# Kernel optimization log

Measured on AMD Instinct MI355X. Metric: run time of the kernel, lower is better.

Reference implementation:

```python
import jax, jax.numpy as jnp
import numpy as np

# Grid / acquisition constants (see input_specs)
NY = NX = 384
NS, NSRC, NREC, NT = 4, 1, 96, 600
DX, DT = 4.0, 0.0005          # from init_kwargs
MAX_VEL = 2500.0              # max_vel passed to scalar()
PML_WIDTH = 20                # PML absorbing-layer width in cells


def setup_inputs() -> dict:
    key = jax.random.key(0)
    k1, k2, k3, k4 = jax.random.split(key, 4)
    # velocity model in [1500, 2500] m/s (consistent with max_vel=2500)
    vp = 1500.0 + 1000.0 * jax.random.uniform(k1, (NY, NX), dtype=jnp.float32)
    src_amp_y = jax.random.normal(k2, (NS, NSRC, NT), dtype=jnp.float32)
    # locations kept inside the interior, away from the PML
    src_loc_y = jax.random.randint(k3, (NS, NSRC, 2), PML_WIDTH + 10, NY - PML_WIDTH - 10).astype(jnp.int32)
    rec_loc_y = jax.random.randint(k4, (NS, NREC, 2), PML_WIDTH + 10, NY - PML_WIDTH - 10).astype(jnp.int32)
    return {"vp": vp, "src_amp_y": src_amp_y, "src_loc_y": src_loc_y, "rec_loc_y": rec_loc_y}


def _pml_sigma_1d(n):
    # quadratic PML damping profile, classic 3*vmax*ln(1000)/(2*L) scaling
    x = jnp.arange(n, dtype=jnp.float32)
    left = jnp.clip((PML_WIDTH - x) / PML_WIDTH, 0.0)
    right = jnp.clip((x - (n - 1 - PML_WIDTH)) / PML_WIDTH, 0.0)
    d0 = 3.0 * MAX_VEL * np.log(1000.0) / (2.0 * PML_WIDTH * DX)
    return d0 * jnp.maximum(left, right) ** 2


def _laplacian(u):
    # 4th-order accurate 2D Laplacian, zero (Dirichlet) padding; u: [S, ny, nx]
    c0, c1, c2 = -1.0 / 12.0, 4.0 / 3.0, -5.0 / 2.0
    up = jnp.pad(u, ((0, 0), (2, 2), (2, 2)))
    ly = (c0 * (up[:, :-4, 2:-2] + up[:, 4:, 2:-2])
          + c1 * (up[:, 1:-3, 2:-2] + up[:, 3:-1, 2:-2])
          + c2 * up[:, 2:-2, 2:-2])
    lx = (c0 * (up[:, 2:-2, :-4] + up[:, 2:-2, 4:])
          + c1 * (up[:, 2:-2, 1:-3] + up[:, 2:-2, 3:-1])
          + c2 * up[:, 2:-2, 2:-2])
    return (ly + lx) / (DX * DX)


def _propagate(vp, src_amp_y, src_loc_y, rec_loc_y):
    S = src_amp_y.shape[0]
    v2dt2 = (vp * vp) * (DT * DT)                     # [ny, nx]
    sigma = _pml_sigma_1d(NY)[:, None] + _pml_sigma_1d(NX)[None, :]
    a = 1.0 + 0.5 * DT * sigma                        # damped leapfrog denominators
    b = 1.0 - 0.5 * DT * sigma

    sy, sx = src_loc_y[..., 0], src_loc_y[..., 1]     # [S, nsrc]
    ry, rx = rec_loc_y[..., 0], rec_loc_y[..., 1]     # [S, nrec]
    shot_s = jnp.broadcast_to(jnp.arange(S)[:, None], sy.shape)
    shot_r = jnp.broadcast_to(jnp.arange(S)[:, None], ry.shape)
    src_scale = v2dt2[sy, sx]                         # [S, nsrc]

    def step(carry, amp_t):
        u_prev, u_cur = carry
        lap = _laplacian(u_cur)
        u_next = (2.0 * u_cur - b * u_prev + v2dt2 * lap) / a
        u_next = u_next.at[shot_s, sy, sx].add(amp_t * src_scale)
        rec = u_next[shot_r, ry, rx]                  # [S, nrec]
        return (u_cur, u_next), rec

    u0 = jnp.zeros((S, NY, NX), dtype=vp.dtype)
    amp_ts = jnp.transpose(src_amp_y, (2, 0, 1))      # [nt, S, nsrc]
    _, recs = jax.lax.scan(step, (u0, u0), amp_ts)
    return jnp.transpose(recs, (1, 2, 0))             # [S, nrec, nt]


def reference(vp, src_amp_y, src_loc_y, rec_loc_y):
    return _propagate(vp, src_amp_y, src_loc_y, rec_loc_y)
```

## Files before the change

kernel.cpp:

```cpp
#include <hip/hip_runtime.h>

constexpr int NY = 384, NX = 384, S = 4, NREC = 96, NT = 600;
constexpr int K = 8;
constexpr int T = 48;
constexpr int L = 80;
constexpr int PAD = 16;
constexpr int PX = NX + 2 * PAD;
constexpr int PNN = PX * PX;
constexpr int TB = NX / T;
constexpr int SP = 84;
constexpr int NPAIR = (L / 2) * (L / 4);
constexpr int TPB = 512;
constexpr float D0 = 323.80102870228766f;
constexpr float HALF_DT = 0.00025f;
constexpr float DT2 = 2.5e-7f;
constexpr float C0 = -1.0f / 12.0f, C1 = 4.0f / 3.0f, C2 = -2.5f;
constexpr float INV_DX2 = 0.0625f;

__device__ __forceinline__ float sigma_of(int y, int x) {
    float yf = (float)y, xf = (float)x;
    float a = fmaxf((20.0f - yf) / 20.0f, 0.0f);
    float b = fmaxf((yf - 363.0f) / 20.0f, 0.0f);
    float m = fmaxf(a, b);
    float sy = D0 * m * m;
    a = fmaxf((20.0f - xf) / 20.0f, 0.0f);
    b = fmaxf((xf - 363.0f) / 20.0f, 0.0f);
    m = fmaxf(a, b);
    float sx = D0 * m * m;
    return sy + sx;
}

__global__ __launch_bounds__(256) void init_vp(
    const float* __restrict__ vp, float* __restrict__ vppad)
{
    int i = blockIdx.x * 256 + threadIdx.x;
    if (i >= PNN) return;
    int py = i / PX, px = i - py * PX;
    int dy = py - PAD, dx = px - PAD;
    bool in = ((unsigned)dy < (unsigned)NY) && ((unsigned)dx < (unsigned)NX);
    vppad[i] = in ? vp[dy * NX + dx] : 0.0f;
}

__device__ __forceinline__ float4 ld4g(const float* p) { return *(const float4*)p; }
__device__ __forceinline__ void st4g(float* p, float4 v) { *(float4*)p = v; }
__device__ __forceinline__ float get4(const float4& v, int c) {
    return c == 0 ? v.x : c == 1 ? v.y : c == 2 ? v.z : v.w;
}
__device__ __forceinline__ void set4(float4& v, int c, float x) {
    if (c == 0) v.x = x; else if (c == 1) v.y = x; else if (c == 2) v.z = x; else v.w = x;
}

__device__ __forceinline__ void coeff_quad(int gy, int gx, float4 vq,
                                           float4& v2, float4& bb, float4& ia)
{
    v2.x = vq.x * vq.x * DT2; v2.y = vq.y * vq.y * DT2;
    v2.z = vq.z * vq.z * DT2; v2.w = vq.w * vq.w * DT2;
    float s0 = sigma_of(gy, gx),     s1 = sigma_of(gy, gx + 1);
    float s2 = sigma_of(gy, gx + 2), s3 = sigma_of(gy, gx + 3);
    bb.x = 1.0f - HALF_DT * s0; bb.y = 1.0f - HALF_DT * s1;
    bb.z = 1.0f - HALF_DT * s2; bb.w = 1.0f - HALF_DT * s3;
    float a0 = 1.0f + HALF_DT * s0, a1 = 1.0f + HALF_DT * s1;
    float a2 = 1.0f + HALF_DT * s2, a3 = 1.0f + HALF_DT * s3;
    bool iny = ((unsigned)gy < (unsigned)NY);
    ia.x = (iny && (unsigned)gx < (unsigned)NX)       ? 1.0f / a0 : 0.0f;
    ia.y = (iny && (unsigned)(gx + 1) < (unsigned)NX) ? 1.0f / a1 : 0.0f;
    ia.z = (iny && (unsigned)(gx + 2) < (unsigned)NX) ? 1.0f / a2 : 0.0f;
    ia.w = (iny && (unsigned)(gx + 3) < (unsigned)NX) ? 1.0f / a3 : 0.0f;
}

__device__ __forceinline__ float4 quad_update(
    float4 cen, float4 up, float4 v2, float4 bb, float4 ia,
    float4 ym2, float4 ym1, float4 yp1, float4 yp2,
    float xm2a, float xm1a, float xp1a, float xp2a)
{
    float4 r;
    float lyv, lxv, lap;
    lyv = C0 * (ym2.x + yp2.x) + C1 * (ym1.x + yp1.x) + C2 * cen.x;
    lxv = C0 * (xm2a + cen.z) + C1 * (xm1a + cen.y) + C2 * cen.x;
    lap = (lyv + lxv) * INV_DX2;
    r.x = (2.0f * cen.x - bb.x * up.x + v2.x * lap) * ia.x;
    lyv = C0 * (ym2.y + yp2.y) + C1 * (ym1.y + yp1.y) + C2 * cen.y;
    lxv = C0 * (xm1a + cen.w) + C1 * (cen.x + cen.z) + C2 * cen.y;
    lap = (lyv + lxv) * INV_DX2;
    r.y = (2.0f * cen.y - bb.y * up.y + v2.y * lap) * ia.y;
    lyv = C0 * (ym2.z + yp2.z) + C1 * (ym1.z + yp1.z) + C2 * cen.z;
    lxv = C0 * (cen.x + xp1a) + C1 * (cen.y + cen.w) + C2 * cen.z;
    lap = (lyv + lxv) * INV_DX2;
    r.z = (2.0f * cen.z - bb.z * up.z + v2.z * lap) * ia.z;
    lyv = C0 * (ym2.w + yp2.w) + C1 * (ym1.w + yp1.w) + C2 * cen.w;
    lxv = C0 * (cen.y + xp2a) + C1 * (cen.z + xp1a) + C2 * cen.w;
    lap = (lyv + lxv) * INV_DX2;
    r.w = (2.0f * cen.w - bb.w * up.w + v2.w * lap) * ia.w;
    return r;
}

__device__ __forceinline__ void pair_step(
    const float* __restrict__ Ain, float* __restrict__ Aout,
    int m, int rl, int qc4, float aj,
    float4& cenL, float4& cenU, float4& upL, float4& upU,
    const float4& v2L, const float4& v2U, const float4& bbL, const float4& bbU,
    const float4& iaL, const float4& iaU, const float4& saL, const float4& saU)
{
    if (rl < m || rl >= L - m || qc4 + 3 < m || qc4 >= L - m) return;
    const int b = rl * SP + qc4;
    float4 rm2 = *(const float4*)&Ain[b - 2 * SP];
    float4 rm1 = *(const float4*)&Ain[b - SP];
    float4 rp2 = *(const float4*)&Ain[b + 2 * SP];
    float4 rp3 = *(const float4*)&Ain[b + 3 * SP];
    float2 xmL = *(const float2*)&Ain[b - 2];
    float2 xpL = *(const float2*)&Ain[b + 4];
    float2 xmU = *(const float2*)&Ain[b + SP - 2];
    float2 xpU = *(const float2*)&Ain[b + SP + 4];
    float4 rL = quad_update(cenL, upL, v2L, bbL, iaL, rm2, rm1, cenU, rp2,
                            xmL.x, xmL.y, xpL.x, xpL.y);
    float4 rU = quad_update(cenU, upU, v2U, bbU, iaU, rm1, cenL, rp2, rp3,
                            xmU.x, xmU.y, xpU.x, xpU.y);
    rL.x += aj * saL.x; rL.y += aj * saL.y; rL.z += aj * saL.z; rL.w += aj * saL.w;
    rU.x += aj * saU.x; rU.y += aj * saU.y; rU.z += aj * saU.z; rU.w += aj * saU.w;
    *(float4*)&Aout[b] = rL;
    *(float4*)&Aout[b + SP] = rU;
    upL = cenL; cenL = rL;
    upU = cenU; cenU = rU;
}

__device__ __forceinline__ void slot_setup(
    int p, int py0, int px0, int gy0, int gx0, int sly, int slx, bool has_src,
    const float* __restrict__ upIn, const float* __restrict__ ucIn,
    const float* __restrict__ vppad, float* __restrict__ A0,
    int& rl, int& qc4,
    float4& cenL, float4& cenU, float4& upL, float4& upU,
    float4& v2L, float4& v2U, float4& bbL, float4& bbU,
    float4& iaL, float4& iaU, float4& saL, float4& saU)
{
    int pr = p / 20;
    qc4 = (p - pr * 20) * 4;
    rl = 2 * pr;
    int pa = (py0 + rl) * PX + px0 + qc4;
    upL = ld4g(upIn + pa);        upU = ld4g(upIn + pa + PX);
    cenL = ld4g(ucIn + pa);       cenU = ld4g(ucIn + pa + PX);
    *(float4*)&A0[rl * SP + qc4] = cenL;
    *(float4*)&A0[(rl + 1) * SP + qc4] = cenU;
    float4 vqL = ld4g(vppad + pa), vqU = ld4g(vppad + pa + PX);
    int gy = gy0 + rl, gx = gx0 + qc4;
    coeff_quad(gy,     gx, vqL, v2L, bbL, iaL);
    coeff_quad(gy + 1, gx, vqU, v2U, bbU, iaU);
    saL = make_float4(0.f, 0.f, 0.f, 0.f); saU = saL;
    if (has_src && slx >= qc4 && slx < qc4 + 4) {
        int c = slx - qc4;
        if (sly == rl)          set4(saL, c, get4(v2L, c));
        else if (sly == rl + 1) set4(saU, c, get4(v2U, c));
    }
}

__global__ __launch_bounds__(TPB) void stepK(
    float* __restrict__ ubuf,
    const float* __restrict__ vppad,
    const float* __restrict__ src_amp,
    const int* __restrict__ src_loc,
    const int* __restrict__ rec_loc,
    float* __restrict__ out,
    int t0, int pin, int pout)
{
    __shared__ __align__(16) float A0[SP * L];
    __shared__ __align__(16) float A1[SP * L];
    __shared__ int r_lidx[NREC];
    __shared__ int r_tout[NREC];
    __shared__ int r_cnt;

    const int tid = threadIdx.x;
    const int bx = blockIdx.x, by = blockIdx.y, s = blockIdx.z;

    const float* upIn = ubuf + (size_t)(s * 4 + pin) * PNN;
    const float* ucIn = upIn + PNN;
    float* upOut = ubuf + (size_t)(s * 4 + pout) * PNN;
    float* ucOut = upOut + PNN;

    const int py0 = by * T;
    const int px0 = bx * T;
    const int gy0 = py0 - PAD;
    const int gx0 = px0 - PAD;

    if (tid == 0) r_cnt = 0;

    const int sy = src_loc[2 * s], sx = src_loc[2 * s + 1];
    const int sly = sy - gy0, slx = sx - gx0;
    const bool has_src = ((unsigned)sly < (unsigned)L) && ((unsigned)slx < (unsigned)L);
    const float4 a0 = ld4g(&src_amp[s * NT + t0]);
    const float4 a1 = ld4g(&src_amp[s * NT + t0 + 4]);

    const bool act1 = (tid < NPAIR - TPB);
    int rl0, qc40, rl1 = 2, qc41 = 0;
    float4 cenL0, cenU0, upL0, upU0, v2L0, v2U0, bbL0, bbU0, iaL0, iaU0, saL0, saU0;
    float4 cenL1 = {}, cenU1 = {}, upL1 = {}, upU1 = {}, v2L1 = {}, v2U1 = {},
           bbL1 = {}, bbU1 = {}, iaL1 = {}, iaU1 = {}, saL1 = {}, saU1 = {};

    slot_setup(tid, py0, px0, gy0, gx0, sly, slx, has_src, upIn, ucIn, vppad, A0,
               rl0, qc40, cenL0, cenU0, upL0, upU0, v2L0, v2U0, bbL0, bbU0,
               iaL0, iaU0, saL0, saU0);
    if (act1)
        slot_setup(tid + TPB, py0, px0, gy0, gx0, sly, slx, has_src, upIn, ucIn, vppad, A0,
                   rl1, qc41, cenL1, cenU1, upL1, upU1, v2L1, v2U1, bbL1, bbU1,
                   iaL1, iaU1, saL1, saU1);
    __syncthreads();

    if (tid < NREC) {
        int r = s * NREC + tid;
        int ry = rec_loc[2 * r], rx = rec_loc[2 * r + 1];
        if (ry >= by * T && ry < by * T + T && rx >= bx * T && rx < bx * T + T) {
            int k = atomicAdd(&r_cnt, 1);
            r_lidx[k] = (ry - gy0) * SP + (rx - gx0);
            r_tout[k] = r * NT + t0;
        }
    }

#pragma unroll
    for (int j = 0; j < K; ++j) {
        const int m = 2 * (j + 1);
        const float* Ain = (j & 1) ? A1 : A0;
        float* Aout = (j & 1) ? A0 : A1;
        const float aj = (j == 0) ? a0.x : (j == 1) ? a0.y : (j == 2) ? a0.z :
                         (j == 3) ? a0.w : (j == 4) ? a1.x : (j == 5) ? a1.y :
                         (j == 6) ? a1.z : a1.w;
        pair_step(Ain, Aout, m, rl0, qc40, aj, cenL0, cenU0, upL0, upU0,
                  v2L0, v2U0, bbL0, bbU0, iaL0, iaU0, saL0, saU0);
        if (act1)
            pair_step(Ain, Aout, m, rl1, qc41, aj, cenL1, cenU1, upL1, upU1,
                      v2L1, v2U1, bbL1, bbU1, iaL1, iaU1, saL1, saU1);
        __syncthreads();
        if (tid < r_cnt) out[r_tout[tid] + j] = Aout[r_lidx[tid]];
    }

    if (rl0 >= PAD && rl0 < L - PAD && qc40 >= PAD && qc40 < L - PAD) {
        int pa = (py0 + rl0) * PX + px0 + qc40;
        st4g(ucOut + pa, cenL0);       st4g(upOut + pa, upL0);
        st4g(ucOut + pa + PX, cenU0);  st4g(upOut + pa + PX, upU0);
    }
    if (act1 && rl1 >= PAD && rl1 < L - PAD && qc41 >= PAD && qc41 < L - PAD) {
        int pa = (py0 + rl1) * PX + px0 + qc41;
        st4g(ucOut + pa, cenL1);       st4g(upOut + pa, upL1);
        st4g(ucOut + pa + PX, cenU1);  st4g(upOut + pa + PX, upU1);
    }
}

extern "C" void kernel_launch(void* const* d_in, const int* in_sizes, int n_in,
                              void* d_out, int out_size, void* d_ws, size_t ws_size,
                              hipStream_t stream)
{
    const float* vp      = (const float*)d_in[0];
    const float* src_amp = (const float*)d_in[1];
    const int*   src_loc = (const int*)d_in[2];
    const int*   rec_loc = (const int*)d_in[3];
    float* out = (float*)d_out;

    float* ws = (float*)d_ws;
    float* vppad = ws;
    float* ubuf  = vppad + PNN;

    hipMemsetAsync(ubuf, 0, (size_t)S * 4 * PNN * sizeof(float), stream);
    init_vp<<<(PNN + 255) / 256, 256, 0, stream>>>(vp, vppad);

    for (int l = 0; l < NT / K; ++l) {
        int pin = (l & 1) ? 2 : 0;
        int pout = (l & 1) ? 0 : 2;
        stepK<<<dim3(TB, TB, S), TPB, 0, stream>>>(
            ubuf, vppad, src_amp, src_loc, rec_loc, out,
            l * K, pin, pout);
    }
}
```

Measured before the change: 960.6 us.

## Skip tiles outside the source light cone and precompute coefficient tables

```diff
diff --git a/kernel.cpp b/kernel.cpp
--- a/kernel.cpp
+++ b/kernel.cpp
@@ -17,28 +17,26 @@
 constexpr float C0 = -1.0f / 12.0f, C1 = 4.0f / 3.0f, C2 = -2.5f;
 constexpr float INV_DX2 = 0.0625f;
 
-__device__ __forceinline__ float sigma_of(int y, int x) {
-    float yf = (float)y, xf = (float)x;
-    float a = fmaxf((20.0f - yf) / 20.0f, 0.0f);
-    float b = fmaxf((yf - 363.0f) / 20.0f, 0.0f);
-    float m = fmaxf(a, b);
-    float sy = D0 * m * m;
-    a = fmaxf((20.0f - xf) / 20.0f, 0.0f);
-    b = fmaxf((xf - 363.0f) / 20.0f, 0.0f);
-    m = fmaxf(a, b);
-    float sx = D0 * m * m;
-    return sy + sx;
-}
-
-__global__ __launch_bounds__(256) void init_vp(
-    const float* __restrict__ vp, float* __restrict__ vppad)
+__device__ __forceinline__ float sig1d(int d) {
+    float f = (float)d;
+    float l = fmaxf((20.0f - f) / 20.0f, 0.0f);
+    float r = fmaxf((f - 363.0f) / 20.0f, 0.0f);
+    float m = fmaxf(l, r);
+    return D0 * m * m;
+}
+
+__global__ __launch_bounds__(256) void init_all(
+    const float* __restrict__ vp,
+    float* __restrict__ v2p, float* __restrict__ sig1)
 {
     int i = blockIdx.x * 256 + threadIdx.x;
     if (i >= PNN) return;
     int py = i / PX, px = i - py * PX;
     int dy = py - PAD, dx = px - PAD;
     bool in = ((unsigned)dy < (unsigned)NY) && ((unsigned)dx < (unsigned)NX);
-    vppad[i] = in ? vp[dy * NX + dx] : 0.0f;
+    float v = in ? vp[dy * NX + dx] : 0.0f;
+    v2p[i] = v * v * DT2;
+    if (i < PX) sig1[i] = sig1d(i - PAD);
 }
 
 __device__ __forceinline__ float4 ld4g(const float* p) { return *(const float4*)p; }
@@ -50,22 +48,24 @@
     if (c == 0) v.x = x; else if (c == 1) v.y = x; else if (c == 2) v.z = x; else v.w = x;
 }
 
-__device__ __forceinline__ void coeff_quad(int gy, int gx, float4 vq,
-                                           float4& v2, float4& bb, float4& ia)
-{
-    v2.x = vq.x * vq.x * DT2; v2.y = vq.y * vq.y * DT2;
-    v2.z = vq.z * vq.z * DT2; v2.w = vq.w * vq.w * DT2;
-    float s0 = sigma_of(gy, gx),     s1 = sigma_of(gy, gx + 1);
-    float s2 = sigma_of(gy, gx + 2), s3 = sigma_of(gy, gx + 3);
-    bb.x = 1.0f - HALF_DT * s0; bb.y = 1.0f - HALF_DT * s1;
-    bb.z = 1.0f - HALF_DT * s2; bb.w = 1.0f - HALF_DT * s3;
-    float a0 = 1.0f + HALF_DT * s0, a1 = 1.0f + HALF_DT * s1;
-    float a2 = 1.0f + HALF_DT * s2, a3 = 1.0f + HALF_DT * s3;
-    bool iny = ((unsigned)gy < (unsigned)NY);
-    ia.x = (iny && (unsigned)gx < (unsigned)NX)       ? 1.0f / a0 : 0.0f;
-    ia.y = (iny && (unsigned)(gx + 1) < (unsigned)NX) ? 1.0f / a1 : 0.0f;
-    ia.z = (iny && (unsigned)(gx + 2) < (unsigned)NX) ? 1.0f / a2 : 0.0f;
-    ia.w = (iny && (unsigned)(gx + 3) < (unsigned)NX) ? 1.0f / a3 : 0.0f;
+__device__ __forceinline__ float nr_rcp(float a) {
+    float r = __builtin_amdgcn_rcpf(a);
+    r = r * (2.0f - a * r);
+    r = r * (2.0f - a * r);
+    return r;
+}
+
+__device__ __forceinline__ void coeff_quad_tab(float syv, float4 sx4,
+                                               bool iny, int gx,
+                                               float4& bb, float4& ia)
+{
+    float h0 = HALF_DT * (syv + sx4.x), h1 = HALF_DT * (syv + sx4.y);
+    float h2 = HALF_DT * (syv + sx4.z), h3 = HALF_DT * (syv + sx4.w);
+    bb.x = 1.0f - h0; bb.y = 1.0f - h1; bb.z = 1.0f - h2; bb.w = 1.0f - h3;
+    ia.x = (iny && (unsigned)gx < (unsigned)NX)       ? nr_rcp(1.0f + h0) : 0.0f;
+    ia.y = (iny && (unsigned)(gx + 1) < (unsigned)NX) ? nr_rcp(1.0f + h1) : 0.0f;
+    ia.z = (iny && (unsigned)(gx + 2) < (unsigned)NX) ? nr_rcp(1.0f + h2) : 0.0f;
+    ia.w = (iny && (unsigned)(gx + 3) < (unsigned)NX) ? nr_rcp(1.0f + h3) : 0.0f;
 }
 
 __device__ __forceinline__ float4 quad_update(
@@ -126,7 +126,8 @@
 __device__ __forceinline__ void slot_setup(
     int p, int py0, int px0, int gy0, int gx0, int sly, int slx, bool has_src,
     const float* __restrict__ upIn, const float* __restrict__ ucIn,
-    const float* __restrict__ vppad, float* __restrict__ A0,
+    const float* __restrict__ v2p, const float* __restrict__ sig1,
+    float* __restrict__ A0,
     int& rl, int& qc4,
     float4& cenL, float4& cenU, float4& upL, float4& upU,
     float4& v2L, float4& v2U, float4& bbL, float4& bbU,
@@ -140,10 +141,12 @@
     cenL = ld4g(ucIn + pa);       cenU = ld4g(ucIn + pa + PX);
     *(float4*)&A0[rl * SP + qc4] = cenL;
     *(float4*)&A0[(rl + 1) * SP + qc4] = cenU;
-    float4 vqL = ld4g(vppad + pa), vqU = ld4g(vppad + pa + PX);
+    v2L = ld4g(v2p + pa);         v2U = ld4g(v2p + pa + PX);
+    float syL = sig1[py0 + rl], syU = sig1[py0 + rl + 1];
+    float4 sx4 = ld4g(sig1 + px0 + qc4);
     int gy = gy0 + rl, gx = gx0 + qc4;
-    coeff_quad(gy,     gx, vqL, v2L, bbL, iaL);
-    coeff_quad(gy + 1, gx, vqU, v2U, bbU, iaU);
+    coeff_quad_tab(syL, sx4, (unsigned)gy < (unsigned)NY,       gx, bbL, iaL);
+    coeff_quad_tab(syU, sx4, (unsigned)(gy + 1) < (unsigned)NY, gx, bbU, iaU);
     saL = make_float4(0.f, 0.f, 0.f, 0.f); saU = saL;
     if (has_src && slx >= qc4 && slx < qc4 + 4) {
         int c = slx - qc4;
@@ -154,7 +157,7 @@
 
 __global__ __launch_bounds__(TPB) void stepK(
     float* __restrict__ ubuf,
-    const float* __restrict__ vppad,
+    const float* __restrict__ v2p, const float* __restrict__ sig1,
     const float* __restrict__ src_amp,
     const int* __restrict__ src_loc,
     const int* __restrict__ rec_loc,
@@ -180,9 +183,27 @@
     const int gy0 = py0 - PAD;
     const int gx0 = px0 - PAD;
 
+    const int sy = src_loc[2 * s], sx = src_loc[2 * s + 1];
+
+    {
+        int ddy = max(0, max(gy0 - sy, sy - (gy0 + L - 1)));
+        int ddx = max(0, max(gx0 - sx, sx - (gx0 + L - 1)));
+        if (ddy + ddx > 2 * (t0 + K) + 2) {
+            if (tid < NREC) {
+                int r = s * NREC + tid;
+                int ry = rec_loc[2 * r], rx = rec_loc[2 * r + 1];
+                if (ry >= by * T && ry < by * T + T &&
+                    rx >= bx * T && rx < bx * T + T) {
+#pragma unroll
+                    for (int j = 0; j < K; ++j) out[r * NT + t0 + j] = 0.0f;
+                }
+            }
+            return;
+        }
+    }
+
     if (tid == 0) r_cnt = 0;
 
-    const int sy = src_loc[2 * s], sx = src_loc[2 * s + 1];
     const int sly = sy - gy0, slx = sx - gx0;
     const bool has_src = ((unsigned)sly < (unsigned)L) && ((unsigned)slx < (unsigned)L);
     const float4 a0 = ld4g(&src_amp[s * NT + t0]);
@@ -194,11 +215,11 @@
     float4 cenL1 = {}, cenU1 = {}, upL1 = {}, upU1 = {}, v2L1 = {}, v2U1 = {},
            bbL1 = {}, bbU1 = {}, iaL1 = {}, iaU1 = {}, saL1 = {}, saU1 = {};
 
-    slot_setup(tid, py0, px0, gy0, gx0, sly, slx, has_src, upIn, ucIn, vppad, A0,
+    slot_setup(tid, py0, px0, gy0, gx0, sly, slx, has_src, upIn, ucIn, v2p, sig1, A0,
                rl0, qc40, cenL0, cenU0, upL0, upU0, v2L0, v2U0, bbL0, bbU0,
                iaL0, iaU0, saL0, saU0);
     if (act1)
-        slot_setup(tid + TPB, py0, px0, gy0, gx0, sly, slx, has_src, upIn, ucIn, vppad, A0,
+        slot_setup(tid + TPB, py0, px0, gy0, gx0, sly, slx, has_src, upIn, ucIn, v2p, sig1, A0,
                    rl1, qc41, cenL1, cenU1, upL1, upU1, v2L1, v2U1, bbL1, bbU1,
                    iaL1, iaU1, saL1, saU1);
     __syncthreads();
@@ -253,17 +274,18 @@
     float* out = (float*)d_out;
 
     float* ws = (float*)d_ws;
-    float* vppad = ws;
-    float* ubuf  = vppad + PNN;
+    float* v2p  = ws;
+    float* sig1 = v2p + PNN;
+    float* ubuf = sig1 + PX;
 
     hipMemsetAsync(ubuf, 0, (size_t)S * 4 * PNN * sizeof(float), stream);
-    init_vp<<<(PNN + 255) / 256, 256, 0, stream>>>(vp, vppad);
+    init_all<<<(PNN + 255) / 256, 256, 0, stream>>>(vp, v2p, sig1);
 
     for (int l = 0; l < NT / K; ++l) {
         int pin = (l & 1) ? 2 : 0;
         int pout = (l & 1) ? 0 : 2;
         stepK<<<dim3(TB, TB, S), TPB, 0, stream>>>(
-            ubuf, vppad, src_amp, src_loc, rec_loc, out,
+            ubuf, v2p, sig1, src_amp, src_loc, rec_loc, out,
             l * K, pin, pout);
     }
 }
```

New measurement: 880.6 us. 8.3% less time.
